# Optimization experiments

Measured on AMD Instinct MI355X. Metric: run time of the kernel, lower is better.

The kernel has to match this reference:

```python
import jax, jax.numpy as jnp
import numpy as np

CHUNK = 64  # output-column tile to bound the [M, K, CHUNK] intermediate


def _mam(A, B):
    """Multiply-and-max/min 'matmul': C[m,n] = max_k(A[m,k]*B[k,n]) + min_k(A[m,k]*B[k,n]).
    A: [M, K], B: [K, N]. Tiled over N to avoid materializing [M, K, N]."""
    M, K = A.shape
    N = B.shape[1]
    assert N % CHUNK == 0
    # [N/CHUNK, K, CHUNK]
    B_tiles = B.reshape(K, N // CHUNK, CHUNK).transpose(1, 0, 2)

    def step(carry, B_blk):
        # prod: [M, K, CHUNK]
        prod = A[:, :, None] * B_blk[None, :, :]
        out = prod.max(axis=1) + prod.min(axis=1)  # [M, CHUNK]
        return carry, out

    _, tiles = jax.lax.scan(step, 0, B_tiles)  # [N/CHUNK, M, CHUNK]
    return tiles.transpose(1, 0, 2).reshape(M, N)


def setup_inputs() -> dict:
    key = jax.random.key(0)
    k1, k2, k3 = jax.random.split(key, 3)
    M, K, N = 2048, 1024, 1024
    x = jax.random.normal(k1, (M, K), dtype=jnp.float32)
    # torch stores weight as [out_features, in_features]
    weight = jax.random.normal(k2, (N, K), dtype=jnp.float32) * (1.0 / np.sqrt(K))
    bias = jax.random.normal(k3, (N,), dtype=jnp.float32) * (1.0 / np.sqrt(K))
    return {"x": x, "weight": weight, "bias": bias}


def reference(x, weight, bias):
    # beta == 0 (beta=False): forward is MAM(x, W^T) + bias
    C = _mam(x, weight.T)
    return C + bias[None, :]
```

## Files before the change

kernel.cpp:

```cpp
#include <hip/hip_runtime.h>
#include <math.h>


#define BM 64
#define BN 64
#define BK 32
#define LDSW 68

__device__ __forceinline__ void mam_update(float& mx, float& mn, float p0, float p1) {
    float nmx, nmn;
    asm("v_max3_f32 %0, %1, %2, %3" : "=v"(nmx) : "v"(p0), "v"(p1), "v"(mx));
    asm("v_min3_f32 %0, %1, %2, %3" : "=v"(nmn) : "v"(p0), "v"(p1), "v"(mn));
    mx = nmx;
    mn = nmn;
}

__global__ __launch_bounds__(256) void mam_kernel(
    const float* __restrict__ A,
    const float* __restrict__ W,
    const float* __restrict__ bias,
    float* __restrict__ C,
    int M, int N, int K)
{
    __shared__ float As[BK][LDSW];
    __shared__ float Ws[BK][LDSW];

    const int t  = threadIdx.x;
    const int tx = t & 15;
    const int ty = t >> 4;
    const int m0 = blockIdx.y * BM;
    const int n0 = blockIdx.x * BN;

    const int r  = t >> 3;
    const int kq = t & 7;

    const float* Aptr = A + (size_t)(m0 + r) * K + kq * 4;
    const float* Wptr = W + (size_t)(n0 + r) * K + kq * 4;

    float vmax[4][4], vmin[4][4];
#pragma unroll
    for (int i = 0; i < 4; ++i)
#pragma unroll
        for (int j = 0; j < 4; ++j) {
            vmax[i][j] = -INFINITY;
            vmin[i][j] =  INFINITY;
        }

    for (int k0 = 0; k0 < K; k0 += BK) {
        float4 a0 = *(const float4*)(Aptr);
        float4 a1 = *(const float4*)(Aptr + (size_t)32 * K);
        float4 w0 = *(const float4*)(Wptr);
        float4 w1 = *(const float4*)(Wptr + (size_t)32 * K);
        Aptr += BK;
        Wptr += BK;

        const int kk = kq * 4;
        As[kk + 0][r]      = a0.x;
        As[kk + 1][r]      = a0.y;
        As[kk + 2][r]      = a0.z;
        As[kk + 3][r]      = a0.w;
        As[kk + 0][r + 32] = a1.x;
        As[kk + 1][r + 32] = a1.y;
        As[kk + 2][r + 32] = a1.z;
        As[kk + 3][r + 32] = a1.w;

        Ws[kk + 0][r]      = w0.x;
        Ws[kk + 1][r]      = w0.y;
        Ws[kk + 2][r]      = w0.z;
        Ws[kk + 3][r]      = w0.w;
        Ws[kk + 0][r + 32] = w1.x;
        Ws[kk + 1][r + 32] = w1.y;
        Ws[kk + 2][r + 32] = w1.z;
        Ws[kk + 3][r + 32] = w1.w;

        __syncthreads();

#pragma unroll
        for (int k = 0; k < BK; k += 2) {
            float4 ta0 = *(const float4*)&As[k    ][ty * 4];
            float4 ta1 = *(const float4*)&As[k + 1][ty * 4];
            float4 tb0 = *(const float4*)&Ws[k    ][tx * 4];
            float4 tb1 = *(const float4*)&Ws[k + 1][tx * 4];

            float a0v[4], a1v[4], b0v[4], b1v[4];
            a0v[0] = ta0.x; a0v[1] = ta0.y; a0v[2] = ta0.z; a0v[3] = ta0.w;
            a1v[0] = ta1.x; a1v[1] = ta1.y; a1v[2] = ta1.z; a1v[3] = ta1.w;
            b0v[0] = tb0.x; b0v[1] = tb0.y; b0v[2] = tb0.z; b0v[3] = tb0.w;
            b1v[0] = tb1.x; b1v[1] = tb1.y; b1v[2] = tb1.z; b1v[3] = tb1.w;

#pragma unroll
            for (int i = 0; i < 4; ++i) {
#pragma unroll
                for (int j = 0; j < 4; ++j) {
                    float p0 = a0v[i] * b0v[j];
                    float p1 = a1v[i] * b1v[j];
                    mam_update(vmax[i][j], vmin[i][j], p0, p1);
                }
            }
        }

        __syncthreads();
    }

    float4 bv = *(const float4*)(bias + n0 + tx * 4);
    float bvv[4] = {bv.x, bv.y, bv.z, bv.w};
#pragma unroll
    for (int i = 0; i < 4; ++i) {
        float4 o;
        o.x = vmax[i][0] + vmin[i][0] + bvv[0];
        o.y = vmax[i][1] + vmin[i][1] + bvv[1];
        o.z = vmax[i][2] + vmin[i][2] + bvv[2];
        o.w = vmax[i][3] + vmin[i][3] + bvv[3];
        *(float4*)(C + (size_t)(m0 + ty * 4 + i) * N + n0 + tx * 4) = o;
    }
}

extern "C" void kernel_launch(void* const* d_in, const int* in_sizes, int n_in,
                              void* d_out, int out_size, void* d_ws, size_t ws_size,
                              hipStream_t stream) {
    const float* x    = (const float*)d_in[0];
    const float* w    = (const float*)d_in[1];
    const float* bias = (const float*)d_in[2];
    float* out = (float*)d_out;

    const int N = in_sizes[2];
    const int K = in_sizes[1] / N;
    const int M = in_sizes[0] / K;

    dim3 grid(N / BN, M / BM);
    dim3 block(256);
    mam_kernel<<<grid, block, 0, stream>>>(x, w, bias, out, M, N, K);
}
```

Before: 172.2 us.

## Restructure MAM kernel around transposed A and scalar-broadcast packed multiplies

Adds a pre-pass that transposes A into a k-major float4 workspace. The main kernel then has each thread own one output row and eight columns. Weight pairs are read as uniform 64-bit scalars and multiplied with v_pk_mul_f32 against per-thread A pairs, so shared memory and barriers are gone and the multiplies use packed math with double-buffered register prefetch. This costs an extra kernel launch, a full pass over A, and a dependence on scalar loads of W, and the fast path is hard-wired to K==1024. The old tiled kernel remains as a fallback.

```diff
diff --git a/kernel.cpp b/kernel.cpp
--- a/kernel.cpp
+++ b/kernel.cpp
@@ -1,13 +1,130 @@
 #include <hip/hip_runtime.h>
 #include <math.h>
 
+
+typedef float f32x2 __attribute__((ext_vector_type(2)));
+
+static __device__ __forceinline__ f32x2 pkmul_sv(f32x2 a, double w) {
+    f32x2 d;
+    asm("v_pk_mul_f32 %0, %1, %2" : "=v"(d) : "v"(a), "s"(w));
+    return d;
+}
+static __device__ __forceinline__ void upd(float& mx, float& mn, f32x2 p) {
+    float nmx, nmn;
+    asm("v_max3_f32 %0, %1, %2, %3" : "=v"(nmx) : "v"(p.x), "v"(p.y), "v"(mx));
+    asm("v_min3_f32 %0, %1, %2, %3" : "=v"(nmn) : "v"(p.x), "v"(p.y), "v"(mn));
+    mx = nmx;
+    mn = nmn;
+}
+
+__global__ __launch_bounds__(256) void transpose_a(
+    const float* __restrict__ A, float4* __restrict__ at4, int M, int K)
+{
+    __shared__ float4 T[16][65];
+    const int t = threadIdx.x;
+    const int r = t >> 3;
+    const int c = t & 7;
+    const int m0 = blockIdx.y * 64;
+    const int k0 = blockIdx.x * 64;
+
+    const float4* Ar0 = (const float4*)(A + (size_t)(m0 + r) * K + k0);
+    const float4* Ar1 = (const float4*)(A + (size_t)(m0 + r + 32) * K + k0);
+    T[c][r]          = Ar0[c];
+    T[c + 8][r]      = Ar0[c + 8];
+    T[c][r + 32]     = Ar1[c];
+    T[c + 8][r + 32] = Ar1[c + 8];
+    __syncthreads();
+
+    const int ml = t & 63;
+    const int jq = t >> 6;
+    const int j0 = blockIdx.x * 16;
+#pragma unroll
+    for (int q = 0; q < 4; ++q) {
+        const int jl = jq * 4 + q;
+        at4[(size_t)(j0 + jl) * M + m0 + ml] = T[jl][ml];
+    }
+}
+
+__global__ __launch_bounds__(256) void mam_main(
+    const float4* __restrict__ at4, const float* __restrict__ W,
+    const float* __restrict__ bias, float* __restrict__ C,
+    int M, int N, int K)
+{
+    const int t  = threadIdx.x;
+    const int m  = blockIdx.y * 256 + t;
+    const int n0 = blockIdx.x * 8;
+    const int J  = K >> 2;
+    const int Kd = K >> 1;
+    const double* Wd = (const double*)W;
+
+    float mx[8], mn[8];
+#pragma unroll
+    for (int i = 0; i < 8; ++i) { mx[i] = -INFINITY; mn[i] = INFINITY; }
+
+    const char* aBase = (const char*)(at4 + m);
+    const int aStride = M * 16;
+
+    f32x2  aL[2], aH[2];
+    double w01[2][8], w23[2][8];
+#pragma unroll
+    for (int b = 0; b < 2; ++b) {
+        aL[b] = *(const f32x2*)(aBase + (size_t)b * aStride);
+        aH[b] = *(const f32x2*)(aBase + (size_t)b * aStride + 8);
+#pragma unroll
+        for (int n = 0; n < 8; ++n) {
+            w01[b][n] = Wd[(size_t)(n0 + n) * Kd + 2 * b];
+            w23[b][n] = Wd[(size_t)(n0 + n) * Kd + 2 * b + 1];
+        }
+    }
+
+#pragma unroll 2
+    for (int j = 0; j < 254; ++j) {
+        const int b = j & 1;
+        const f32x2 al = aL[b], ah = aH[b];
+#pragma unroll
+        for (int n = 0; n < 8; ++n) {
+            upd(mx[n], mn[n], pkmul_sv(al, w01[b][n]));
+            upd(mx[n], mn[n], pkmul_sv(ah, w23[b][n]));
+        }
+        aL[b] = *(const f32x2*)(aBase + (size_t)(j + 2) * aStride);
+        aH[b] = *(const f32x2*)(aBase + (size_t)(j + 2) * aStride + 8);
+#pragma unroll
+        for (int n = 0; n < 8; ++n) {
+            w01[b][n] = Wd[(size_t)(n0 + n) * Kd + 2 * (j + 2)];
+            w23[b][n] = Wd[(size_t)(n0 + n) * Kd + 2 * (j + 2) + 1];
+        }
+    }
+#pragma unroll
+    for (int j = 254; j < 256; ++j) {
+        const int b = j & 1;
+        const f32x2 al = aL[b], ah = aH[b];
+#pragma unroll
+        for (int n = 0; n < 8; ++n) {
+            upd(mx[n], mn[n], pkmul_sv(al, w01[b][n]));
+            upd(mx[n], mn[n], pkmul_sv(ah, w23[b][n]));
+        }
+    }
+
+    float4 o0, o1;
+    o0.x = mx[0] + mn[0] + bias[n0 + 0];
+    o0.y = mx[1] + mn[1] + bias[n0 + 1];
+    o0.z = mx[2] + mn[2] + bias[n0 + 2];
+    o0.w = mx[3] + mn[3] + bias[n0 + 3];
+    o1.x = mx[4] + mn[4] + bias[n0 + 4];
+    o1.y = mx[5] + mn[5] + bias[n0 + 5];
+    o1.z = mx[6] + mn[6] + bias[n0 + 6];
+    o1.w = mx[7] + mn[7] + bias[n0 + 7];
+    float4* Crow = (float4*)(C + (size_t)m * N + n0);
+    Crow[0] = o0;
+    Crow[1] = o1;
+}
 
 #define BM 64
 #define BN 64
 #define BK 32
 #define LDSW 68
 
-__device__ __forceinline__ void mam_update(float& mx, float& mn, float p0, float p1) {
+__device__ __forceinline__ void mam_update_fb(float& mx, float& mn, float p0, float p1) {
     float nmx, nmn;
     asm("v_max3_f32 %0, %1, %2, %3" : "=v"(nmx) : "v"(p0), "v"(p1), "v"(mx));
     asm("v_min3_f32 %0, %1, %2, %3" : "=v"(nmn) : "v"(p0), "v"(p1), "v"(mn));
@@ -15,11 +132,9 @@
     mn = nmn;
 }
 
-__global__ __launch_bounds__(256) void mam_kernel(
-    const float* __restrict__ A,
-    const float* __restrict__ W,
-    const float* __restrict__ bias,
-    float* __restrict__ C,
+__global__ __launch_bounds__(256) void mam_fallback(
+    const float* __restrict__ A, const float* __restrict__ W,
+    const float* __restrict__ bias, float* __restrict__ C,
     int M, int N, int K)
 {
     __shared__ float As[BK][LDSW];
@@ -30,7 +145,6 @@
     const int ty = t >> 4;
     const int m0 = blockIdx.y * BM;
     const int n0 = blockIdx.x * BN;
-
     const int r  = t >> 3;
     const int kq = t & 7;
 
@@ -82,35 +196,31 @@
             float4 tb0 = *(const float4*)&Ws[k    ][tx * 4];
             float4 tb1 = *(const float4*)&Ws[k + 1][tx * 4];
 
-            float a0v[4], a1v[4], b0v[4], b1v[4];
-            a0v[0] = ta0.x; a0v[1] = ta0.y; a0v[2] = ta0.z; a0v[3] = ta0.w;
-            a1v[0] = ta1.x; a1v[1] = ta1.y; a1v[2] = ta1.z; a1v[3] = ta1.w;
-            b0v[0] = tb0.x; b0v[1] = tb0.y; b0v[2] = tb0.z; b0v[3] = tb0.w;
-            b1v[0] = tb1.x; b1v[1] = tb1.y; b1v[2] = tb1.z; b1v[3] = tb1.w;
-
-#pragma unroll
-            for (int i = 0; i < 4; ++i) {
+            float a0v[4] = {ta0.x, ta0.y, ta0.z, ta0.w};
+            float a1v[4] = {ta1.x, ta1.y, ta1.z, ta1.w};
+            float b0v[4] = {tb0.x, tb0.y, tb0.z, tb0.w};
+            float b1v[4] = {tb1.x, tb1.y, tb1.z, tb1.w};
+
+#pragma unroll
+            for (int i = 0; i < 4; ++i)
 #pragma unroll
                 for (int j = 0; j < 4; ++j) {
                     float p0 = a0v[i] * b0v[j];
                     float p1 = a1v[i] * b1v[j];
-                    mam_update(vmax[i][j], vmin[i][j], p0, p1);
+                    mam_update_fb(vmax[i][j], vmin[i][j], p0, p1);
                 }
-            }
-        }
-
+        }
         __syncthreads();
     }
 
     float4 bv = *(const float4*)(bias + n0 + tx * 4);
-    float bvv[4] = {bv.x, bv.y, bv.z, bv.w};
 #pragma unroll
     for (int i = 0; i < 4; ++i) {
         float4 o;
-        o.x = vmax[i][0] + vmin[i][0] + bvv[0];
-        o.y = vmax[i][1] + vmin[i][1] + bvv[1];
-        o.z = vmax[i][2] + vmin[i][2] + bvv[2];
-        o.w = vmax[i][3] + vmin[i][3] + bvv[3];
+        o.x = vmax[i][0] + vmin[i][0] + bv.x;
+        o.y = vmax[i][1] + vmin[i][1] + bv.y;
+        o.z = vmax[i][2] + vmin[i][2] + bv.z;
+        o.w = vmax[i][3] + vmin[i][3] + bv.w;
         *(float4*)(C + (size_t)(m0 + ty * 4 + i) * N + n0 + tx * 4) = o;
     }
 }
@@ -127,7 +237,18 @@
     const int K = in_sizes[1] / N;
     const int M = in_sizes[0] / K;
 
-    dim3 grid(N / BN, M / BM);
-    dim3 block(256);
-    mam_kernel<<<grid, block, 0, stream>>>(x, w, bias, out, M, N, K);
-}
+    const size_t need = (size_t)M * K * sizeof(float);
+    const bool fast_ok = (ws_size >= need) && (K % 64 == 0) && (M % 256 == 0) &&
+                         (N % 8 == 0) && (K == 1024);
+
+    if (fast_ok) {
+        float4* at4 = (float4*)d_ws;
+        dim3 tg(K / 64, M / 64);
+        transpose_a<<<tg, 256, 0, stream>>>(x, at4, M, K);
+        dim3 mg(N / 8, M / 256);
+        mam_main<<<mg, 256, 0, stream>>>(at4, w, bias, out, M, N, K);
+    } else {
+        dim3 grid(N / BN, M / BM);
+        mam_fallback<<<grid, 256, 0, stream>>>(x, w, bias, out, M, N, K);
+    }
+}
```

Measured after the change: 219.2 us. +27.3%, slower.

## Pre-transpose weights into k4-interleaved layout and stream W from registers

Applied to the files above, without the earlier changes.

A small kernel first repacks the weight matrix in the workspace into a layout where each float4 holds four consecutive k values for one output column. The main kernel then reads weights straight from global memory into a double-buffered register prefetch instead of staging them through LDS, and keeps only A in shared memory. This halves LDS traffic and shared-memory footprint per block. In exchange it adds a transpose launch on every call and replaces coalesced LDS reads of W with per-thread global loads. A hardcoded bound (jg < 254) ties the fast path to K == 1024, with the old kernel kept as a fallback.

```diff
diff --git a/kernel.cpp b/kernel.cpp
--- a/kernel.cpp
+++ b/kernel.cpp
@@ -2,12 +2,10 @@
 #include <math.h>
 
 
-#define BM 64
-#define BN 64
 #define BK 32
-#define LDSW 68
-
-__device__ __forceinline__ void mam_update(float& mx, float& mn, float p0, float p1) {
+#define LDSA 68
+
+__device__ __forceinline__ void mam_upd(float& mx, float& mn, float p0, float p1) {
     float nmx, nmn;
     asm("v_max3_f32 %0, %1, %2, %3" : "=v"(nmx) : "v"(p0), "v"(p1), "v"(mx));
     asm("v_min3_f32 %0, %1, %2, %3" : "=v"(nmn) : "v"(p0), "v"(p1), "v"(mn));
@@ -15,27 +13,54 @@
     mn = nmn;
 }
 
-__global__ __launch_bounds__(256) void mam_kernel(
-    const float* __restrict__ A,
-    const float* __restrict__ W,
-    const float* __restrict__ bias,
-    float* __restrict__ C,
+__global__ __launch_bounds__(256) void transpose_k4(
+    const float* __restrict__ X, float4* __restrict__ out, int R, int K)
+{
+    __shared__ float4 T[16][65];
+    const int t = threadIdx.x;
+    const int r = t >> 3;
+    const int c = t & 7;
+    const int r0 = blockIdx.y * 64;
+    const int k0 = blockIdx.x * 64;
+
+    const float4* Xr0 = (const float4*)(X + (size_t)(r0 + r) * K + k0);
+    const float4* Xr1 = (const float4*)(X + (size_t)(r0 + r + 32) * K + k0);
+    T[c][r]          = Xr0[c];
+    T[c + 8][r]      = Xr0[c + 8];
+    T[c][r + 32]     = Xr1[c];
+    T[c + 8][r + 32] = Xr1[c + 8];
+    __syncthreads();
+
+    const int rl = t & 63;
+    const int jq = t >> 6;
+    const int j0 = blockIdx.x * 16;
+#pragma unroll
+    for (int q = 0; q < 4; ++q) {
+        const int jl = jq * 4 + q;
+        out[(size_t)(j0 + jl) * R + r0 + rl] = T[jl][rl];
+    }
+}
+
+__global__ __launch_bounds__(256) void mam_hybrid(
+    const float* __restrict__ A, const float4* __restrict__ wt4,
+    const float* __restrict__ bias, float* __restrict__ C,
     int M, int N, int K)
 {
-    __shared__ float As[BK][LDSW];
-    __shared__ float Ws[BK][LDSW];
+    __shared__ float As[BK][LDSA];
 
     const int t  = threadIdx.x;
     const int tx = t & 15;
     const int ty = t >> 4;
-    const int m0 = blockIdx.y * BM;
-    const int n0 = blockIdx.x * BN;
+    const int m0 = blockIdx.y * 64;
+    const int n0 = blockIdx.x * 64;
 
     const int r  = t >> 3;
     const int kq = t & 7;
 
     const float* Aptr = A + (size_t)(m0 + r) * K + kq * 4;
-    const float* Wptr = W + (size_t)(n0 + r) * K + kq * 4;
+
+    const float4* wp = wt4 + n0 + tx * 4;
+    const int J = K >> 2;
 
     float vmax[4][4], vmin[4][4];
 #pragma unroll
@@ -46,13 +71,18 @@
             vmin[i][j] =  INFINITY;
         }
 
-    for (int k0 = 0; k0 < K; k0 += BK) {
+    float4 wb[2][4];
+#pragma unroll
+    for (int c = 0; c < 4; ++c) {
+        wb[0][c] = wp[c];
+        wb[1][c] = wp[(size_t)N + c];
+    }
+
+    int jg = 0;
+    for (int s = 0; s < K / BK; ++s) {
         float4 a0 = *(const float4*)(Aptr);
         float4 a1 = *(const float4*)(Aptr + (size_t)32 * K);
-        float4 w0 = *(const float4*)(Wptr);
-        float4 w1 = *(const float4*)(Wptr + (size_t)32 * K);
         Aptr += BK;
-        Wptr += BK;
 
         const int kk = kq * 4;
         As[kk + 0][r]      = a0.x;
@@ -64,39 +94,49 @@
         As[kk + 2][r + 32] = a1.z;
         As[kk + 3][r + 32] = a1.w;
 
-        Ws[kk + 0][r]      = w0.x;
-        Ws[kk + 1][r]      = w0.y;
-        Ws[kk + 2][r]      = w0.z;
-        Ws[kk + 3][r]      = w0.w;
-        Ws[kk + 0][r + 32] = w1.x;
-        Ws[kk + 1][r + 32] = w1.y;
-        Ws[kk + 2][r + 32] = w1.z;
-        Ws[kk + 3][r + 32] = w1.w;
-
-        __syncthreads();
-
-#pragma unroll
-        for (int k = 0; k < BK; k += 2) {
-            float4 ta0 = *(const float4*)&As[k    ][ty * 4];
-            float4 ta1 = *(const float4*)&As[k + 1][ty * 4];
-            float4 tb0 = *(const float4*)&Ws[k    ][tx * 4];
-            float4 tb1 = *(const float4*)&Ws[k + 1][tx * 4];
-
-            float a0v[4], a1v[4], b0v[4], b1v[4];
-            a0v[0] = ta0.x; a0v[1] = ta0.y; a0v[2] = ta0.z; a0v[3] = ta0.w;
-            a1v[0] = ta1.x; a1v[1] = ta1.y; a1v[2] = ta1.z; a1v[3] = ta1.w;
-            b0v[0] = tb0.x; b0v[1] = tb0.y; b0v[2] = tb0.z; b0v[3] = tb0.w;
-            b1v[0] = tb1.x; b1v[1] = tb1.y; b1v[2] = tb1.z; b1v[3] = tb1.w;
-
-#pragma unroll
-            for (int i = 0; i < 4; ++i) {
-#pragma unroll
-                for (int j = 0; j < 4; ++j) {
-                    float p0 = a0v[i] * b0v[j];
-                    float p1 = a1v[i] * b1v[j];
-                    mam_update(vmax[i][j], vmin[i][j], p0, p1);
+        __syncthreads();
+
+#pragma unroll
+        for (int jl = 0; jl < BK / 4; ++jl) {
+            const int b = jg & 1;
+            const float4 w0 = wb[b][0];
+            const float4 w1 = wb[b][1];
+            const float4 w2 = wb[b][2];
+            const float4 w3 = wb[b][3];
+
+            if (jg < 254) {
+                const size_t off = (size_t)(jg + 2) * N;
+#pragma unroll
+                for (int c = 0; c < 4; ++c)
+                    wb[b][c] = wp[off + c];
+            }
+
+            const int kb = jl * 4;
+            float4 ta0 = *(const float4*)&As[kb + 0][ty * 4];
+            float4 ta1 = *(const float4*)&As[kb + 1][ty * 4];
+            float4 ta2 = *(const float4*)&As[kb + 2][ty * 4];
+            float4 ta3 = *(const float4*)&As[kb + 3][ty * 4];
+
+            float a0v[4] = {ta0.x, ta0.y, ta0.z, ta0.w};
+            float a1v[4] = {ta1.x, ta1.y, ta1.z, ta1.w};
+            float a2v[4] = {ta2.x, ta2.y, ta2.z, ta2.w};
+            float a3v[4] = {ta3.x, ta3.y, ta3.z, ta3.w};
+
+            const float4 wv[4] = {w0, w1, w2, w3};
+#pragma unroll
+            for (int c = 0; c < 4; ++c) {
+                const float4 w = wv[c];
+#pragma unroll
+                for (int i = 0; i < 4; ++i) {
+                    float p0 = a0v[i] * w.x;
+                    float p1 = a1v[i] * w.y;
+                    mam_upd(vmax[i][c], vmin[i][c], p0, p1);
+                    float p2 = a2v[i] * w.z;
+                    float p3 = a3v[i] * w.w;
+                    mam_upd(vmax[i][c], vmin[i][c], p2, p3);
                 }
             }
+            ++jg;
         }
 
         __syncthreads();
@@ -115,6 +155,103 @@
     }
 }
 
+#define BM 64
+#define BN 64
+#define LDSW 68
+
+__global__ __launch_bounds__(256) void mam_fallback(
+    const float* __restrict__ A, const float* __restrict__ W,
+    const float* __restrict__ bias, float* __restrict__ C,
+    int M, int N, int K)
+{
+    __shared__ float Asf[BK][LDSW];
+    __shared__ float Wsf[BK][LDSW];
+
+    const int t  = threadIdx.x;
+    const int tx = t & 15;
+    const int ty = t >> 4;
+    const int m0 = blockIdx.y * BM;
+    const int n0 = blockIdx.x * BN;
+    const int r  = t >> 3;
+    const int kq = t & 7;
+
+    const float* Aptr = A + (size_t)(m0 + r) * K + kq * 4;
+    const float* Wptr = W + (size_t)(n0 + r) * K + kq * 4;
+
+    float vmax[4][4], vmin[4][4];
+#pragma unroll
+    for (int i = 0; i < 4; ++i)
+#pragma unroll
+        for (int j = 0; j < 4; ++j) {
+            vmax[i][j] = -INFINITY;
+            vmin[i][j] =  INFINITY;
+        }
+
+    for (int k0 = 0; k0 < K; k0 += BK) {
+        float4 a0 = *(const float4*)(Aptr);
+        float4 a1 = *(const float4*)(Aptr + (size_t)32 * K);
+        float4 w0 = *(const float4*)(Wptr);
+        float4 w1 = *(const float4*)(Wptr + (size_t)32 * K);
+        Aptr += BK;
+        Wptr += BK;
+
+        const int kk = kq * 4;
+        Asf[kk + 0][r]      = a0.x;
+        Asf[kk + 1][r]      = a0.y;
+        Asf[kk + 2][r]      = a0.z;
+        Asf[kk + 3][r]      = a0.w;
+        Asf[kk + 0][r + 32] = a1.x;
+        Asf[kk + 1][r + 32] = a1.y;
+        Asf[kk + 2][r + 32] = a1.z;
+        Asf[kk + 3][r + 32] = a1.w;
+
+        Wsf[kk + 0][r]      = w0.x;
+        Wsf[kk + 1][r]      = w0.y;
+        Wsf[kk + 2][r]      = w0.z;
+        Wsf[kk + 3][r]      = w0.w;
+        Wsf[kk + 0][r + 32] = w1.x;
+        Wsf[kk + 1][r + 32] = w1.y;
+        Wsf[kk + 2][r + 32] = w1.z;
+        Wsf[kk + 3][r + 32] = w1.w;
+
+        __syncthreads();
+
+#pragma unroll
+        for (int k = 0; k < BK; k += 2) {
+            float4 ta0 = *(const float4*)&Asf[k    ][ty * 4];
+            float4 ta1 = *(const float4*)&Asf[k + 1][ty * 4];
+            float4 tb0 = *(const float4*)&Wsf[k    ][tx * 4];
+            float4 tb1 = *(const float4*)&Wsf[k + 1][tx * 4];
+
+            float a0v[4] = {ta0.x, ta0.y, ta0.z, ta0.w};
+            float a1v[4] = {ta1.x, ta1.y, ta1.z, ta1.w};
+            float b0v[4] = {tb0.x, tb0.y, tb0.z, tb0.w};
+            float b1v[4] = {tb1.x, tb1.y, tb1.z, tb1.w};
+
+#pragma unroll
+            for (int i = 0; i < 4; ++i)
+#pragma unroll
+                for (int j = 0; j < 4; ++j) {
+                    float p0 = a0v[i] * b0v[j];
+                    float p1 = a1v[i] * b1v[j];
+                    mam_upd(vmax[i][j], vmin[i][j], p0, p1);
+                }
+        }
+        __syncthreads();
+    }
+
+    float4 bv = *(const float4*)(bias + n0 + tx * 4);
+#pragma unroll
+    for (int i = 0; i < 4; ++i) {
+        float4 o;
+        o.x = vmax[i][0] + vmin[i][0] + bv.x;
+        o.y = vmax[i][1] + vmin[i][1] + bv.y;
+        o.z = vmax[i][2] + vmin[i][2] + bv.z;
+        o.w = vmax[i][3] + vmin[i][3] + bv.w;
+        *(float4*)(C + (size_t)(m0 + ty * 4 + i) * N + n0 + tx * 4) = o;
+    }
+}
+
 extern "C" void kernel_launch(void* const* d_in, const int* in_sizes, int n_in,
                               void* d_out, int out_size, void* d_ws, size_t ws_size,
                               hipStream_t stream) {
@@ -127,7 +264,18 @@
     const int K = in_sizes[1] / N;
     const int M = in_sizes[0] / K;
 
-    dim3 grid(N / BN, M / BM);
-    dim3 block(256);
-    mam_kernel<<<grid, block, 0, stream>>>(x, w, bias, out, M, N, K);
-}
+    const size_t needW = (size_t)N * K * sizeof(float);
+    const bool fast_ok = (ws_size >= needW) && (K == 1024) &&
+                         (M % 64 == 0) && (N % 64 == 0);
+
+    if (fast_ok) {
+        float4* wt4 = (float4*)d_ws;
+        dim3 tgw(K / 64, N / 64);
+        transpose_k4<<<tgw, 256, 0, stream>>>(w, wt4, N, K);
+        dim3 mg(N / 64, M / 64);
+        mam_hybrid<<<mg, 256, 0, stream>>>(x, wt4, bias, out, M, N, K);
+    } else {
+        dim3 grid(N / BN, M / BM);
+        mam_fallback<<<grid, 256, 0, stream>>>(x, w, bias, out, M, N, K);
+    }
+}
```

After: 190.0 us. 10.4% more time.
